# Optimization experiments

Hardware: AMD Instinct MI355X
Metric: run time of the kernel (lower is better)

Reference implementation:

```python
import jax, jax.numpy as jnp
import numpy as np

HID = 32          # PositionalEncodingFourier hidden_dim
PE_TEMP = 10000.0


def _layer_norm(x, w, b):
    m = jnp.mean(x, -1, keepdims=True)
    v = jnp.mean((x - m) ** 2, -1, keepdims=True)
    return (x - m) / jnp.sqrt(v + 1e-6) * w + b


def _dwconv(x, w, b):
    # x: (B,C,H,W), w: (C,1,3,3) depthwise
    y = jax.lax.conv_general_dilated(x, w, (1, 1), 'SAME',
                                     feature_group_count=x.shape[1],
                                     dimension_numbers=('NCHW', 'OIHW', 'NCHW'))
    return y + b[None, :, None, None]


def _pos_embed(B, H, W, pw, pb):
    scale = 2 * np.pi
    eps = 1e-6
    dim_t = PE_TEMP ** (2 * (jnp.arange(HID) // 2).astype(jnp.float32) / HID)

    def four(e):  # e: (M,) -> (M,HID), interleaved sin/cos
        p = e[:, None] / dim_t
        return jnp.stack([jnp.sin(p[:, 0::2]), jnp.cos(p[:, 1::2])], -1).reshape(e.shape[0], HID)

    ye = jnp.arange(1, H + 1, dtype=jnp.float32) / (H + eps) * scale
    xe = jnp.arange(1, W + 1, dtype=jnp.float32) / (W + eps) * scale
    py = jnp.broadcast_to(four(ye)[:, None, :], (H, W, HID))
    px = jnp.broadcast_to(four(xe)[None, :, :], (H, W, HID))
    pos = jnp.concatenate([py, px], -1) @ pw.T + pb     # (H,W,C)
    C = pos.shape[-1]
    return jnp.broadcast_to(pos[None], (B, H, W, C)).reshape(B, H * W, C)


def _l2norm(x):
    return x / jnp.maximum(jnp.linalg.norm(x, axis=-1, keepdims=True), 1e-12)


def setup_inputs() -> dict:
    key = jax.random.key(0)
    ks = jax.random.split(key, 10)
    B, C, H, W = 32, 384, 32, 32
    nh, hid = 6, 6 * C
    f32 = jnp.float32
    d = {
        'x': jax.random.normal(ks[0], (B, C, H, W), f32),
        'pos_w': 0.02 * jax.random.normal(ks[1], (C, 2 * HID), f32),
        'pos_b': jnp.zeros((C,), f32),
        'ln1_w': jnp.ones((C,), f32), 'ln1_b': jnp.zeros((C,), f32),
        'q_w': 0.02 * jax.random.normal(ks[2], (C, C), f32), 'q_b': jnp.zeros((C,), f32),
        'k_w': 0.02 * jax.random.normal(ks[3], (C, C), f32), 'k_b': jnp.zeros((C,), f32),
        'vc_w': 0.02 * jax.random.normal(ks[4], (C, C), f32), 'vc_b': jnp.zeros((C,), f32),
        'dw_w': 0.1 * jax.random.normal(ks[5], (C, 1, 3, 3), f32), 'dw_b': jnp.zeros((C,), f32),
        'bn_g': jnp.ones((C,), f32), 'bn_b': jnp.zeros((C,), f32),
        'bn_mean': jnp.zeros((C,), f32), 'bn_var': jnp.ones((C,), f32),
        'temp': jnp.ones((nh, 1, 1), f32),
        'proj_w': 0.02 * jax.random.normal(ks[6], (C, C), f32), 'proj_b': jnp.zeros((C,), f32),
        'gamma1': jnp.full((C,), 1e-6, f32),
        'ln2_w': jnp.ones((C,), f32), 'ln2_b': jnp.zeros((C,), f32),
        'mlp_w1': 0.02 * jax.random.normal(ks[7], (hid, C), f32), 'mlp_b1': jnp.zeros((hid,), f32),
        'mlp_dw': 0.1 * jax.random.normal(ks[8], (hid, 1, 3, 3), f32), 'mlp_db': jnp.zeros((hid,), f32),
        'mlp_w2': 0.02 * jax.random.normal(ks[9], (C, hid), f32), 'mlp_b2': jnp.zeros((C,), f32),
        'gamma2': jnp.full((C,), 1e-6, f32),
    }
    return d


def reference(x, pos_w, pos_b, ln1_w, ln1_b, q_w, q_b, k_w, k_b, vc_w, vc_b,
              dw_w, dw_b, bn_g, bn_b, bn_mean, bn_var, temp, proj_w, proj_b,
              gamma1, ln2_w, ln2_b, mlp_w1, mlp_b1, mlp_dw, mlp_db,
              mlp_w2, mlp_b2, gamma2):
    B, C, H, W = x.shape
    N = H * W
    nh = temp.shape[0]
    dh = C // nh

    xf = x.reshape(B, C, N).transpose(0, 2, 1)          # (B,N,C)
    xf = xf + _pos_embed(B, H, W, pos_w, pos_b)
    xn = _layer_norm(xf, ln1_w, ln1_b)                  # (B,N,C)
    xs = xn.transpose(0, 2, 1).reshape(B, C, H, W)      # spatial view for DWConv

    # --- GLGXCA: channel-wise cross-covariance attention ---
    q = (xn @ q_w.T + q_b).reshape(B, N, nh, dh).transpose(0, 2, 3, 1)  # (B,h,d,N)
    k = (xn @ k_w.T + k_b).reshape(B, N, nh, dh).transpose(0, 2, 3, 1)
    q = _l2norm(q)
    k = _l2norm(k)
    attn = jnp.einsum('bhdn,bhen->bhde', q, k) * temp   # (B,h,d,d)
    attn = jax.nn.softmax(attn, axis=-1)

    vg = _dwconv(xs, dw_w, dw_b)
    vg = (vg - bn_mean[None, :, None, None]) / jnp.sqrt(bn_var + 1e-5)[None, :, None, None] \
         * bn_g[None, :, None, None] + bn_b[None, :, None, None]
    vg = vg * jax.nn.sigmoid(vg)                        # SiLU
    vg = vg.transpose(0, 2, 3, 1).reshape(B, N, C)
    vc = xn @ vc_w.T + vc_b
    v = (vc * vg).reshape(B, N, nh, dh).transpose(0, 2, 3, 1)           # (B,h,d,N)

    xo = jnp.einsum('bhde,bhen->bhdn', attn, v)         # (B,h,d,N)
    xo = xo.transpose(0, 3, 1, 2).reshape(B, N, C)
    xo = xo @ proj_w.T + proj_b
    xo = xo.reshape(B, H, W, C).transpose(0, 3, 1, 2)   # (B,C,H,W)

    # --- residual 1 (faithful: torch does transpose(1,2).reshape on BCHW) ---
    xa = xo * gamma1[None, :, None, None]
    xa = jnp.swapaxes(xa, 1, 2).reshape(B, C, H, W)
    x = x + xa

    # --- MLP branch ---
    xn2 = _layer_norm(x.transpose(0, 2, 3, 1), ln2_w, ln2_b).transpose(0, 3, 1, 2)
    h1 = jnp.einsum('bchw,oc->bohw', xn2, mlp_w1) + mlp_b1[None, :, None, None]
    h1 = jax.nn.gelu(h1, approximate=False)
    h2 = jax.nn.gelu(_dwconv(h1, mlp_dw, mlp_db), approximate=False)
    h3 = jnp.einsum('bchw,oc->bohw', h2, mlp_w2) + mlp_b2[None, :, None, None]
    return x + h3 * gamma2[None, :, None, None]
```

## Files before the change

### kernel.cpp

```cpp
#include <hip/hip_runtime.h>
#include <cstdint>
#include <cstddef>
#include <cmath>

#define DI __device__ __forceinline__

typedef __attribute__((ext_vector_type(2))) float f32x2;
typedef __attribute__((ext_vector_type(4))) float f32x4;
typedef __attribute__((ext_vector_type(8))) __bf16 bf16x8;
typedef __attribute__((ext_vector_type(2))) unsigned short u16x2;
typedef __attribute__((ext_vector_type(4))) unsigned short u16x4;
typedef __attribute__((ext_vector_type(4))) unsigned int u32x4;

constexpr int B_ = 32, C_ = 384, N_ = 1024, HID2_ = 2304, QS_ = 1152;

DI unsigned short f2b(float f) {
  union { float f; unsigned int u; } v; v.f = f;
  unsigned int u = v.u;
  return (unsigned short)((u + 0x7FFFu + ((u >> 16) & 1u)) >> 16);
}
DI float b2f(unsigned short h) {
  union { unsigned int u; float f; } v; v.u = ((unsigned int)h) << 16;
  return v.f;
}
DI float sigmoid_f(float x) { return __builtin_amdgcn_rcpf(1.0f + __expf(-x)); }
DI float gelu_f(float x) { return x * sigmoid_f(1.702f * x); }

DI void gload_lds16(const void* g, void* l) {
  __builtin_amdgcn_global_load_lds(
      (const __attribute__((address_space(1))) void*)g,
      (__attribute__((address_space(3))) void*)l, 16, 0, 0);
}

#if __has_builtin(__builtin_amdgcn_cvt_pk_fp8_f32) && __has_builtin(__builtin_amdgcn_cvt_pk_f32_fp8)
#define HW_FP8 1
#else
#define HW_FP8 0
#endif

DI unsigned char f2e4_sw(float x) {
  float a = fabsf(x);
  unsigned char s = (x < 0.f) ? 0x80 : 0;
  if (!(a >= 0.0009765625f)) return s;
  if (a >= 448.f) return s | 0x7E;
  int e; float m = frexpf(a, &e);
  m *= 2.f; e -= 1;
  if (e < -6) {
    int q = (int)rintf(a * 512.f);
    if (q > 7) return s | 0x08;
    return s | (unsigned char)q;
  }
  int mi = (int)rintf((m - 1.f) * 8.f);
  if (mi == 8) { mi = 0; e += 1; }
  if (e > 8) return s | 0x7E;
  return s | (unsigned char)(((e + 7) << 3) | mi);
}
DI float e42f_sw(unsigned char h) {
  int e = (h >> 3) & 0xF, m = h & 7;
  float v;
  if (e == 0) v = (float)m * 0.001953125f;
  else { union { unsigned u; float f; } w; w.u = (unsigned)((e + 120) << 23) | ((unsigned)m << 20); v = w.f; }
  return (h & 0x80) ? -v : v;
}
DI unsigned char f2e4(float x) {
#if HW_FP8
  int r = __builtin_amdgcn_cvt_pk_fp8_f32(x, x, 0, false);
  return (unsigned char)(r & 0xFF);
#else
  return f2e4_sw(x);
#endif
}
DI unsigned int enc4(float a, float b, float c, float d) {
#if HW_FP8
  int r = 0;
  r = __builtin_amdgcn_cvt_pk_fp8_f32(a, b, r, false);
  r = __builtin_amdgcn_cvt_pk_fp8_f32(c, d, r, true);
  return (unsigned int)r;
#else
  return (unsigned)f2e4(a) | ((unsigned)f2e4(b) << 8) | ((unsigned)f2e4(c) << 16) | ((unsigned)f2e4(d) << 24);
#endif
}
DI void dec4(unsigned int v, float* o) {
#if HW_FP8
  f32x2 lo = __builtin_amdgcn_cvt_pk_f32_fp8((int)v, false);
  f32x2 hi = __builtin_amdgcn_cvt_pk_f32_fp8((int)v, true);
  o[0] = lo[0]; o[1] = lo[1]; o[2] = hi[0]; o[3] = hi[1];
#else
  o[0] = e42f_sw(v & 0xFF); o[1] = e42f_sw((v >> 8) & 0xFF);
  o[2] = e42f_sw((v >> 16) & 0xFF); o[3] = e42f_sw((v >> 24) & 0xFF);
#endif
}

__global__ void prep_k(const float* __restrict__ q_w, const float* __restrict__ k_w,
    const float* __restrict__ vc_w, const float* __restrict__ pj_w,
    const float* __restrict__ w1, const float* __restrict__ w2,
    const float* __restrict__ dw_w, const float* __restrict__ mdw,
    const float* __restrict__ q_b, const float* __restrict__ k_b, const float* __restrict__ v_b,
    unsigned short* __restrict__ WQKV, unsigned short* __restrict__ WP,
    unsigned char* __restrict__ W1, unsigned char* __restrict__ W2,
    float* __restrict__ DT1, float* __restrict__ DT2,
    float* __restrict__ BQKV, float* __restrict__ feat) {
  int i = blockIdx.x * 256 + threadIdx.x;
  if (i < 442368) {
    int o = i / 384, c = i % 384;
    float v = (o < 384) ? q_w[o * 384 + c] : (o < 768) ? k_w[(o - 384) * 384 + c]
                                                       : vc_w[(o - 768) * 384 + c];
    WQKV[i] = f2b(v); return;
  }
  i -= 442368;
  if (i < 147456) { WP[i] = f2b(pj_w[i]); return; }
  i -= 147456;
  if (i < 884736) { W1[i] = f2e4(w1[i]); return; }
  i -= 884736;
  if (i < 884736) { W2[i] = f2e4(w2[i]); return; }
  i -= 884736;
  if (i < 3456)  { int c = i / 9, k = i % 9; DT1[k * C_ + c] = dw_w[i]; return; }
  i -= 3456;
  if (i < 20736) { int c = i / 9, k = i % 9; DT2[k * HID2_ + c] = mdw[i]; return; }
  i -= 20736;
  if (i < 1152)  { BQKV[i] = (i < 384) ? q_b[i] : (i < 768) ? k_b[i - 384] : v_b[i - 768]; return; }
  i -= 1152;
  if (i < 65536) {
    int n = i >> 6, j = i & 63;
    int h = n >> 5, w = n & 31;
    const float scale = 6.283185307179586f;
    float e = (j < 32) ? (float)(h + 1) / (32.0f + 1e-6f) * scale
                       : (float)(w + 1) / (32.0f + 1e-6f) * scale;
    int jj = j & 31;
    float dt = powf(10000.0f, (float)(jj >> 1) * (1.0f / 16.0f));
    float arg = e / dt;
    feat[i] = (jj & 1) ? cosf(arg) : sinf(arg);
  }
}

__global__ __launch_bounds__(384) void pos_k(const float* __restrict__ feat,
    const float* __restrict__ pw, const float* __restrict__ pb, float* __restrict__ pos) {
  __shared__ float fs[64];
  int n = blockIdx.x, c = threadIdx.x;
  if (c < 64) fs[c] = feat[n * 64 + c];
  __syncthreads();
  float s = pb[c];
  #pragma unroll
  for (int j = 0; j < 64; ++j) s += fs[j] * pw[c * 64 + j];
  pos[(size_t)n * C_ + c] = s;
}

template<int HASPOS, int OUT8>
__global__ __launch_bounds__(256) void ln_k(const float* __restrict__ xin,
    const float* __restrict__ pos, const float* __restrict__ lw,
    const float* __restrict__ lb, unsigned short* __restrict__ outb,
    unsigned char* __restrict__ out8) {
  __shared__ float tile[C_ * 33];
  int bid = blockIdx.x;
  int b = bid >> 5, n0 = (bid & 31) << 5;
  int t = threadIdx.x;
  const float* xb = xin + (size_t)b * C_ * N_;
  #pragma unroll
  for (int i = 0; i < 48; ++i) {
    int f = t + 256 * i;
    int c = f >> 5, nn = f & 31;
    tile[c * 33 + nn] = xb[(size_t)c * N_ + n0 + nn];
  }
  __syncthreads();
  int wv = t >> 6, l = t & 63;
  for (int tk = 0; tk < 8; ++tk) {
    int tn = wv * 8 + tk;
    float v[6];
    #pragma unroll
    for (int i = 0; i < 6; ++i) {
      int c = l + 64 * i;
      float x = tile[c * 33 + tn];
      if (HASPOS) x += pos[(size_t)(n0 + tn) * C_ + c];
      v[i] = x;
    }
    float s = v[0] + v[1] + v[2] + v[3] + v[4] + v[5];
    #pragma unroll
    for (int m = 1; m < 64; m <<= 1) s += __shfl_xor(s, m);
    float mean = s * (1.0f / 384.0f);
    float q = 0.f;
    #pragma unroll
    for (int i = 0; i < 6; ++i) { float d = v[i] - mean; q += d * d; }
    #pragma unroll
    for (int m = 1; m < 64; m <<= 1) q += __shfl_xor(q, m);
    float rstd = rsqrtf(q * (1.0f / 384.0f) + 1e-6f);
    #pragma unroll
    for (int i = 0; i < 6; ++i) {
      int c = l + 64 * i;
      float val = (v[i] - mean) * rstd * lw[c] + lb[c];
      if (OUT8) out8[((size_t)b * N_ + n0 + tn) * C_ + c] = f2e4(val);
      else      outb[((size_t)b * N_ + n0 + tn) * C_ + c] = f2b(val);
    }
  }
}

template<int EPI>
__global__ __launch_bounds__(256) void gemm_k(const unsigned short* __restrict__ A,
    const unsigned short* __restrict__ Wt, const float* __restrict__ bias,
    unsigned short* __restrict__ outb, int M, int K, int O) {
  __shared__ __align__(16) unsigned short As[2][128 * 64];
  __shared__ __align__(16) unsigned short Bs[2][128 * 64];
  const int gx = gridDim.x;
  const int nwg = gx * gridDim.y;
  const int lid = blockIdx.y * gx + blockIdx.x;
  const int chunk = nwg >> 3;
  const int swz = (lid & 7) * chunk + (lid >> 3);
  const int m0 = (swz / gx) * 128, n0 = (swz % gx) * 128;
  const int t = threadIdx.x, l = t & 63, wv = t >> 6;
  const int wr = wv >> 1, wc = wv & 1;
  const int fr = l & 15, fq = l >> 4;
  const int arow = t >> 3;
  const int acsw = ((t & 7) ^ (arow & 7)) * 8;
  const unsigned short* Ag = A + (size_t)(m0 + arow) * K + acsw;
  const unsigned short* Bg = Wt + (size_t)(n0 + arow) * K + acsw;
  f32x4 acc[4][4];
  #pragma unroll
  for (int i = 0; i < 4; ++i)
    #pragma unroll
    for (int j = 0; j < 4; ++j) acc[i][j] = f32x4{0.f, 0.f, 0.f, 0.f};

  auto stage = [&](int buf, int k0) {
    char* Ad = (char*)&As[buf][0] + wv * 1024;
    char* Bd = (char*)&Bs[buf][0] + wv * 1024;
    #pragma unroll
    for (int s = 0; s < 4; ++s) {
      gload_lds16(Ag + (size_t)(s * 32) * K + k0, Ad + s * 4096);
      gload_lds16(Bg + (size_t)(s * 32) * K + k0, Bd + s * 4096);
    }
  };

  const int nt = K >> 6;
  stage(0, 0);
  for (int tt = 0; tt < nt; ++tt) {
    const int cur = tt & 1;
    if (tt + 1 < nt) {
      stage(cur ^ 1, (tt + 1) << 6);
      asm volatile("s_waitcnt vmcnt(8)" ::: "memory");
    } else {
      asm volatile("s_waitcnt vmcnt(0)" ::: "memory");
    }
    __builtin_amdgcn_s_barrier();
    #pragma unroll
    for (int kk = 0; kk < 2; ++kk) {
      bf16x8 af[4], bfr[4];
      #pragma unroll
      for (int mi = 0; mi < 4; ++mi) {
        int row = wr * 64 + mi * 16 + fr;
        af[mi] = *(const bf16x8*)((const char*)&As[cur][0] + row * 128 +
                                  ((((kk << 2) | fq) ^ (row & 7)) << 4));
      }
      #pragma unroll
      for (int ni = 0; ni < 4; ++ni) {
        int row = wc * 64 + ni * 16 + fr;
        bfr[ni] = *(const bf16x8*)((const char*)&Bs[cur][0] + row * 128 +
                                   ((((kk << 2) | fq) ^ (row & 7)) << 4));
      }
      #pragma unroll
      for (int mi = 0; mi < 4; ++mi)
        #pragma unroll
        for (int ni = 0; ni < 4; ++ni)
          acc[mi][ni] = __builtin_amdgcn_mfma_f32_16x16x32_bf16(af[mi], bfr[ni], acc[mi][ni], 0, 0, 0);
    }
    __builtin_amdgcn_s_barrier();
  }
  const int rb = fq * 4;
  #pragma unroll
  for (int mi = 0; mi < 4; ++mi) {
    #pragma unroll
    for (int ni = 0; ni < 4; ++ni) {
      int col = n0 + wc * 64 + ni * 16 + fr;
      float bv = bias[col];
      #pragma unroll
      for (int j = 0; j < 4; ++j) {
        int row = m0 + wr * 64 + mi * 16 + rb + j;
        outb[(size_t)row * O + col] = f2b(acc[mi][ni][j] + bv);
      }
    }
  }
}

__global__ __launch_bounds__(256) void fc1_8_k(const unsigned char* __restrict__ A,
    const unsigned char* __restrict__ Wt, const float* __restrict__ bias,
    unsigned char* __restrict__ outb8, int K, int O) {
  __shared__ __align__(16) unsigned char As[2][128 * 128];
  __shared__ __align__(16) unsigned char Bs[2][128 * 128];
  const int gx = gridDim.x;
  const int nwg = gx * gridDim.y;
  const int lid = blockIdx.y * gx + blockIdx.x;
  const int chunk = nwg >> 3;
  const int swz = (lid & 7) * chunk + (lid >> 3);
  const int m0 = (swz / gx) * 128, n0 = (swz % gx) * 128;
  const int t = threadIdx.x, l = t & 63, wv = t >> 6;
  const int wr = wv >> 1, wc = wv & 1;
  const int fr = l & 15, fq = l >> 4;
  const int arow = t >> 3;
  const int acsw = ((t & 7) ^ (arow & 7)) * 16;
  const unsigned char* Ag = A + (size_t)(m0 + arow) * K + acsw;
  const unsigned char* Bg = Wt + (size_t)(n0 + arow) * K + acsw;
  f32x4 acc[4][4];
  #pragma unroll
  for (int i = 0; i < 4; ++i)
    #pragma unroll
    for (int j = 0; j < 4; ++j) acc[i][j] = f32x4{0.f, 0.f, 0.f, 0.f};

  auto stage = [&](int buf, int k0) {
    char* Ad = (char*)&As[buf][0] + wv * 1024;
    char* Bd = (char*)&Bs[buf][0] + wv * 1024;
    #pragma unroll
    for (int s = 0; s < 4; ++s) {
      gload_lds16(Ag + (size_t)(s * 32) * K + k0, Ad + s * 4096);
      gload_lds16(Bg + (size_t)(s * 32) * K + k0, Bd + s * 4096);
    }
  };

  const int nt = K >> 7;
  stage(0, 0);
  for (int tt = 0; tt < nt; ++tt) {
    const int cur = tt & 1;
    if (tt + 1 < nt) {
      stage(cur ^ 1, (tt + 1) << 7);
      asm volatile("s_waitcnt vmcnt(8)" ::: "memory");
    } else {
      asm volatile("s_waitcnt vmcnt(0)" ::: "memory");
    }
    __builtin_amdgcn_s_barrier();
    #pragma unroll
    for (int kk = 0; kk < 4; ++kk) {
      const int slot = (kk << 1) | (fq >> 1);
      const int sub = (fq & 1) << 3;
      long af[4], bfr[4];
      #pragma unroll
      for (int mi = 0; mi < 4; ++mi) {
        int row = wr * 64 + mi * 16 + fr;
        af[mi] = *(const long*)((const char*)&As[cur][0] + row * 128 +
                                ((slot ^ (row & 7)) << 4) + sub);
      }
      #pragma unroll
      for (int ni = 0; ni < 4; ++ni) {
        int row = wc * 64 + ni * 16 + fr;
        bfr[ni] = *(const long*)((const char*)&Bs[cur][0] + row * 128 +
                                 ((slot ^ (row & 7)) << 4) + sub);
      }
      #pragma unroll
      for (int mi = 0; mi < 4; ++mi)
        #pragma unroll
        for (int ni = 0; ni < 4; ++ni)
          acc[mi][ni] = __builtin_amdgcn_mfma_f32_16x16x32_fp8_fp8(af[mi], bfr[ni], acc[mi][ni], 0, 0, 0);
    }
    __builtin_amdgcn_s_barrier();
  }
  const int rb = fq * 4;
  #pragma unroll
  for (int mi = 0; mi < 4; ++mi) {
    #pragma unroll
    for (int ni = 0; ni < 4; ++ni) {
      int col = n0 + wc * 64 + ni * 16 + fr;
      float bv = bias[col];
      #pragma unroll
      for (int j = 0; j < 4; ++j) {
        int row = m0 + wr * 64 + mi * 16 + rb + j;
        outb8[(size_t)row * O + col] = f2e4(gelu_f(acc[mi][ni][j] + bv));
      }
    }
  }
}

__global__ __launch_bounds__(256) void fc2t8_k(const unsigned char* __restrict__ W2b,
    const unsigned char* __restrict__ H2, const float* __restrict__ b2,
    const float* __restrict__ g2, float* __restrict__ out, int bofs) {
  __shared__ __align__(16) unsigned char As[2][128 * 128];
  __shared__ __align__(16) unsigned char Bs[2][128 * 128];
  const int K = HID2_;
  const int nwg = 8 * gridDim.y;
  const int lid = blockIdx.y * 8 + blockIdx.x;
  const int chunk = nwg >> 3;
  const int swz = (lid & 7) * chunk + (lid >> 3);
  const int n0 = (swz & 7) * 128;
  const int y2 = swz >> 3;
  const int img = y2 / 3, m0 = (y2 % 3) * 128;
  const int t = threadIdx.x, l = t & 63, wv = t >> 6;
  const int wr = wv >> 1, wc = wv & 1;
  const int fr = l & 15, fq = l >> 4;
  const int arow = t >> 3;
  const int acsw = ((t & 7) ^ (arow & 7)) * 16;
  const unsigned char* Ag = W2b + (size_t)(m0 + arow) * K + acsw;
  const unsigned char* Bg = H2 + ((size_t)img * N_ + n0 + arow) * K + acsw;
  f32x4 acc[4][4];
  #pragma unroll
  for (int i = 0; i < 4; ++i)
    #pragma unroll
    for (int j = 0; j < 4; ++j) acc[i][j] = f32x4{0.f, 0.f, 0.f, 0.f};

  auto stage = [&](int buf, int k0) {
    char* Ad = (char*)&As[buf][0] + wv * 1024;
    char* Bd = (char*)&Bs[buf][0] + wv * 1024;
    #pragma unroll
    for (int s = 0; s < 4; ++s) {
      gload_lds16(Ag + (size_t)(s * 32) * K + k0, Ad + s * 4096);
      gload_lds16(Bg + (size_t)(s * 32) * K + k0, Bd + s * 4096);
    }
  };

  const int nt = K >> 7;
  stage(0, 0);
  for (int tt = 0; tt < nt; ++tt) {
    const int cur = tt & 1;
    if (tt + 1 < nt) {
      stage(cur ^ 1, (tt + 1) << 7);
      asm volatile("s_waitcnt vmcnt(8)" ::: "memory");
    } else {
      asm volatile("s_waitcnt vmcnt(0)" ::: "memory");
    }
    __builtin_amdgcn_s_barrier();
    #pragma unroll
    for (int kk = 0; kk < 4; ++kk) {
      const int slot = (kk << 1) | (fq >> 1);
      const int sub = (fq & 1) << 3;
      long af[4], bfr[4];
      #pragma unroll
      for (int mi = 0; mi < 4; ++mi) {
        int row = wr * 64 + mi * 16 + fr;
        af[mi] = *(const long*)((const char*)&As[cur][0] + row * 128 +
                                ((slot ^ (row & 7)) << 4) + sub);
      }
      #pragma unroll
      for (int ni = 0; ni < 4; ++ni) {
        int row = wc * 64 + ni * 16 + fr;
        bfr[ni] = *(const long*)((const char*)&Bs[cur][0] + row * 128 +
                                 ((slot ^ (row & 7)) << 4) + sub);
      }
      #pragma unroll
      for (int mi = 0; mi < 4; ++mi)
        #pragma unroll
        for (int ni = 0; ni < 4; ++ni)
          acc[mi][ni] = __builtin_amdgcn_mfma_f32_16x16x32_fp8_fp8(af[mi], bfr[ni], acc[mi][ni], 0, 0, 0);
    }
    __builtin_amdgcn_s_barrier();
  }
  const int rb = fq * 4;
  const size_t obase = ((size_t)(img + bofs) * C_) << 10;
  #pragma unroll
  for (int mi = 0; mi < 4; ++mi) {
    #pragma unroll
    for (int j = 0; j < 4; ++j) {
      int row = m0 + wr * 64 + mi * 16 + rb + j;
      float bv = b2[row], gv = g2[row];
      #pragma unroll
      for (int ni = 0; ni < 4; ++ni) {
        int col = n0 + wc * 64 + ni * 16 + fr;
        size_t oi = obase + ((size_t)row << 10) + col;
        out[oi] = out[oi] + gv * (acc[mi][ni][j] + bv);
      }
    }
  }
}

__global__ __launch_bounds__(256) void attn_k(const unsigned short* __restrict__ qkv,
    const float* __restrict__ temp, unsigned short* __restrict__ attnbf) {
  __shared__ __align__(16) float Qs[32][68];
  __shared__ __align__(16) float Ks[32][68];
  __shared__ float qinv_s[64], kinv_s[64];
  const int bid = blockIdx.x;
  const int b = bid / 6, h = bid % 6;
  const int t = threadIdx.x;
  const unsigned short* qb = qkv + (size_t)b * N_ * QS_ + h * 64;
  const unsigned short* kb = qb + 384;
  const int li = t >> 4, ld = (t & 15) * 4;
  const int d0 = (t >> 4) * 4, e0 = (t & 15) * 4;
  float acc[4][4] = {};
  float ssq = 0.0f;
  for (int n0 = 0; n0 < N_; n0 += 32) {
    __syncthreads();
    #pragma unroll
    for (int rr = 0; rr < 2; ++rr) {
      int i = li + rr * 16;
      u16x4 qv = *(const u16x4*)(qb + (size_t)(n0 + i) * QS_ + ld);
      u16x4 kv = *(const u16x4*)(kb + (size_t)(n0 + i) * QS_ + ld);
      #pragma unroll
      for (int j = 0; j < 4; ++j) { Qs[i][ld + j] = b2f(qv[j]); Ks[i][ld + j] = b2f(kv[j]); }
    }
    __syncthreads();
    if (t < 64) {
      #pragma unroll
      for (int i = 0; i < 32; ++i) { float x = Qs[i][t]; ssq += x * x; }
    } else if (t < 128) {
      #pragma unroll
      for (int i = 0; i < 32; ++i) { float x = Ks[i][t - 64]; ssq += x * x; }
    }
    #pragma unroll
    for (int i = 0; i < 32; ++i) {
      f32x4 qv = *(const f32x4*)&Qs[i][d0];
      f32x4 kv = *(const f32x4*)&Ks[i][e0];
      #pragma unroll
      for (int di = 0; di < 4; ++di)
        #pragma unroll
        for (int ei = 0; ei < 4; ++ei) acc[di][ei] += qv[di] * kv[ei];
    }
  }
  if (t < 64) { float nr = sqrtf(ssq); qinv_s[t] = 1.0f / fmaxf(nr, 1e-12f); }
  else if (t < 128) { float nr = sqrtf(ssq); kinv_s[t - 64] = 1.0f / fmaxf(nr, 1e-12f); }
  __syncthreads();
  const float tp = temp[h];
  #pragma unroll
  for (int di = 0; di < 4; ++di) {
    int d = d0 + di;
    float vals[4];
    #pragma unroll
    for (int ei = 0; ei < 4; ++ei) vals[ei] = acc[di][ei] * qinv_s[d] * kinv_s[e0 + ei] * tp;
    float mx = fmaxf(fmaxf(vals[0], vals[1]), fmaxf(vals[2], vals[3]));
    #pragma unroll
    for (int m = 1; m < 16; m <<= 1) mx = fmaxf(mx, __shfl_xor(mx, m));
    float ex[4], s = 0.f;
    #pragma unroll
    for (int ei = 0; ei < 4; ++ei) { ex[ei] = __expf(vals[ei] - mx); s += ex[ei]; }
    #pragma unroll
    for (int m = 1; m < 16; m <<= 1) s += __shfl_xor(s, m);
    float inv = __builtin_amdgcn_rcpf(s);
    u16x4 ov;
    #pragma unroll
    for (int ei = 0; ei < 4; ++ei) ov[ei] = f2b(ex[ei] * inv);
    *(u16x4*)(attnbf + ((size_t)(b * 6 + h) * 64 + d) * 64 + e0) = ov;
  }
}

__global__ __launch_bounds__(192) void dwconv1_k(const unsigned short* __restrict__ xn,
    const float* __restrict__ dwt, const float* __restrict__ dwb,
    const float* __restrict__ bng, const float* __restrict__ bnb,
    const float* __restrict__ bnm, const float* __restrict__ bnv,
    unsigned short* __restrict__ qkv) {
  const int c0 = threadIdx.x * 4;
  const int h = blockIdx.y >> 2;
  const int w0 = (blockIdx.y & 3) * 8 + threadIdx.y * 4;
  const int b = blockIdx.z;
  const unsigned short* xb = xn + ((size_t)b * N_ + h * 32) * C_ + c0;
  f32x4 acc[4] = {};
  #pragma unroll
  for (int dy = -1; dy <= 1; ++dy) {
    int hh = h + dy;
    if (hh < 0 || hh >= 32) continue;
    f32x4 xf[6];
    #pragma unroll
    for (int j = 0; j < 6; ++j) {
      int ww = w0 - 1 + j;
      if (ww >= 0 && ww < 32) {
        u16x4 xv = *(const u16x4*)(xb + (dy * 32 + ww) * C_);
        xf[j] = f32x4{b2f(xv[0]), b2f(xv[1]), b2f(xv[2]), b2f(xv[3])};
      } else xf[j] = f32x4{0.f, 0.f, 0.f, 0.f};
    }
    #pragma unroll
    for (int dx = 0; dx < 3; ++dx) {
      f32x4 wv = *(const f32x4*)(dwt + ((dy + 1) * 3 + dx) * C_ + c0);
      #pragma unroll
      for (int px = 0; px < 4; ++px)
        #pragma unroll
        for (int j = 0; j < 4; ++j) acc[px][j] += xf[dx + px][j] * wv[j];
    }
  }
  f32x4 dbv = *(const f32x4*)(dwb + c0);
  f32x4 mv = *(const f32x4*)(bnm + c0);
  f32x4 vv = *(const f32x4*)(bnv + c0);
  f32x4 gv = *(const f32x4*)(bng + c0);
  f32x4 bv = *(const f32x4*)(bnb + c0);
  f32x4 rs;
  #pragma unroll
  for (int j = 0; j < 4; ++j) rs[j] = rsqrtf(vv[j] + 1e-5f);
  unsigned short* vb = qkv + ((size_t)b * N_ + h * 32 + w0) * QS_ + 768 + c0;
  #pragma unroll
  for (int px = 0; px < 4; ++px) {
    u16x4 vcv = *(const u16x4*)(vb + px * QS_);
    u16x4 ov;
    #pragma unroll
    for (int j = 0; j < 4; ++j) {
      float u = (acc[px][j] + dbv[j] - mv[j]) * rs[j] * gv[j] + bv[j];
      float si = u * sigmoid_f(u);
      ov[j] = f2b(si * b2f(vcv[j]));
    }
    *(u16x4*)(vb + px * QS_) = ov;
  }
}

__global__ __launch_bounds__(256) void xo_k(const unsigned short* __restrict__ qkv,
    const unsigned short* __restrict__ attn, unsigned short* __restrict__ xo) {
  const int bid = blockIdx.x;
  const int b = bid / 96, r = bid % 96, h = r / 16, m0 = (r % 16) * 64;
  const int t = threadIdx.x, wv = t >> 6, l = t & 63;
  const int n0 = m0 + wv * 16;
  const int fr = l & 15, fk = (l >> 4) * 8;
  const unsigned short* vb = qkv + (size_t)b * N_ * QS_ + 768 + h * 64;
  const unsigned short* ab = attn + (size_t)(b * 6 + h) * 4096;
  f32x4 acc[4];
  #pragma unroll
  for (int i = 0; i < 4; ++i) acc[i] = f32x4{0.f, 0.f, 0.f, 0.f};
  #pragma unroll
  for (int k0 = 0; k0 < 64; k0 += 32) {
    bf16x8 af = *(const bf16x8*)(vb + (size_t)(n0 + fr) * QS_ + k0 + fk);
    #pragma unroll
    for (int ni = 0; ni < 4; ++ni) {
      bf16x8 bfr = *(const bf16x8*)(ab + (ni * 16 + fr) * 64 + k0 + fk);
      acc[ni] = __builtin_amdgcn_mfma_f32_16x16x32_bf16(af, bfr, acc[ni], 0, 0, 0);
    }
  }
  const int rb = (l >> 4) * 4;
  #pragma unroll
  for (int ni = 0; ni < 4; ++ni)
    #pragma unroll
    for (int j = 0; j < 4; ++j) {
      int row = n0 + rb + j;
      xo[((size_t)b * N_ + row) * C_ + h * 64 + ni * 16 + fr] = f2b(acc[ni][j]);
    }
}

__global__ __launch_bounds__(256) void resid1_k(const float* __restrict__ x,
    const unsigned short* __restrict__ y, const float* __restrict__ g1,
    float* __restrict__ xnew) {
  __shared__ unsigned short yp[32][36];
  __shared__ float g1s[32];
  const int bid = blockIdx.x;
  const int b = bid / C_, c2 = bid % C_;
  const int hsrc = c2 / 12, cs0 = (c2 % 12) * 32;
  const int t = threadIdx.x;
  {
    int wq = t >> 3, h4 = (t & 7) * 4;
    u16x4 vv = *(const u16x4*)(y + ((size_t)b * N_ + hsrc * 32 + wq) * C_ + cs0 + h4);
    *(u16x4*)&yp[wq][h4] = vv;
  }
  if (t < 32) g1s[t] = g1[cs0 + t];
  __syncthreads();
  int h2 = t >> 3, w0 = (t & 7) * 4;
  size_t base = (((size_t)b * C_ + c2) << 10) + h2 * 32 + w0;
  f32x4 xv = *(const f32x4*)(x + base);
  f32x4 ov;
  #pragma unroll
  for (int i = 0; i < 4; ++i) ov[i] = xv[i] + g1s[h2] * b2f(yp[w0 + i][h2]);
  *(f32x4*)(xnew + base) = ov;
}

__global__ __launch_bounds__(192) void dwconv2_k(const unsigned char* __restrict__ h1,
    const float* __restrict__ dwt, const float* __restrict__ dwb,
    unsigned char* __restrict__ h2) {
  const int c0 = (blockIdx.x * 192 + threadIdx.x) * 4;
  const int h = blockIdx.y >> 3, w0 = (blockIdx.y & 7) * 4;
  const int b = blockIdx.z;
  const unsigned char* xb = h1 + ((size_t)b * N_ + h * 32) * HID2_ + c0;
  f32x4 acc[4] = {};
  #pragma unroll
  for (int dy = -1; dy <= 1; ++dy) {
    int hh = h + dy;
    if (hh < 0 || hh >= 32) continue;
    f32x4 xf[6];
    #pragma unroll
    for (int j = 0; j < 6; ++j) {
      int ww = w0 - 1 + j;
      if (ww >= 0 && ww < 32) {
        unsigned int xv = *(const unsigned int*)(xb + (dy * 32 + ww) * HID2_);
        float d4[4]; dec4(xv, d4);
        xf[j] = f32x4{d4[0], d4[1], d4[2], d4[3]};
      } else xf[j] = f32x4{0.f, 0.f, 0.f, 0.f};
    }
    #pragma unroll
    for (int dx = 0; dx < 3; ++dx) {
      f32x4 wv = *(const f32x4*)(dwt + ((dy + 1) * 3 + dx) * HID2_ + c0);
      #pragma unroll
      for (int px = 0; px < 4; ++px)
        #pragma unroll
        for (int j = 0; j < 4; ++j) acc[px][j] += xf[dx + px][j] * wv[j];
    }
  }
  f32x4 dbv = *(const f32x4*)(dwb + c0);
  unsigned char* ob = h2 + ((size_t)b * N_ + h * 32 + w0) * HID2_ + c0;
  #pragma unroll
  for (int px = 0; px < 4; ++px) {
    unsigned int ov = enc4(gelu_f(acc[px][0] + dbv[0]), gelu_f(acc[px][1] + dbv[1]),
                           gelu_f(acc[px][2] + dbv[2]), gelu_f(acc[px][3] + dbv[3]));
    *(unsigned int*)(ob + px * HID2_) = ov;
  }
}

extern "C" void kernel_launch(void* const* d_in, const int* in_sizes, int n_in,
                              void* d_out, int out_size, void* d_ws, size_t ws_size,
                              hipStream_t stream) {
  (void)in_sizes; (void)n_in; (void)out_size;
  const float* x    = (const float*)d_in[0];
  const float* posw = (const float*)d_in[1];
  const float* posb = (const float*)d_in[2];
  const float* ln1w = (const float*)d_in[3];
  const float* ln1b = (const float*)d_in[4];
  const float* q_w  = (const float*)d_in[5];
  const float* q_b  = (const float*)d_in[6];
  const float* k_w  = (const float*)d_in[7];
  const float* k_b  = (const float*)d_in[8];
  const float* v_w  = (const float*)d_in[9];
  const float* v_b  = (const float*)d_in[10];
  const float* dw_w = (const float*)d_in[11];
  const float* dw_b = (const float*)d_in[12];
  const float* bn_g = (const float*)d_in[13];
  const float* bn_b = (const float*)d_in[14];
  const float* bn_m = (const float*)d_in[15];
  const float* bn_v = (const float*)d_in[16];
  const float* temp = (const float*)d_in[17];
  const float* pj_w = (const float*)d_in[18];
  const float* pj_b = (const float*)d_in[19];
  const float* g1   = (const float*)d_in[20];
  const float* ln2w = (const float*)d_in[21];
  const float* ln2b = (const float*)d_in[22];
  const float* w1   = (const float*)d_in[23];
  const float* b1   = (const float*)d_in[24];
  const float* mdw  = (const float*)d_in[25];
  const float* mdb  = (const float*)d_in[26];
  const float* w2   = (const float*)d_in[27];
  const float* b2   = (const float*)d_in[28];
  const float* g2   = (const float*)d_in[29];
  float* out = (float*)d_out;

  char* ws = (char*)d_ws;
  size_t off = 0;
  auto alloc = [&](size_t bytes) { size_t o = off; off += (bytes + 255) & ~(size_t)255; return o; };
  const size_t TOK = (size_t)B_ * N_;
  const size_t BNC2 = TOK * C_ * 2;

  size_t oWQKV = alloc(442368 * 2), oWP = alloc(147456 * 2);
  size_t oW1 = alloc(884736), oW2 = alloc(884736);
  size_t oDT1 = alloc(9 * C_ * 4), oDT2 = alloc(9 * HID2_ * 4);
  size_t oBQKV = alloc(1152 * 4);
  size_t oFEAT = alloc(65536 * 4);
  size_t oPOS  = alloc((size_t)N_ * C_ * 4);
  size_t oATT  = alloc((size_t)B_ * 6 * 4096 * 2);
  size_t oXN2  = alloc(TOK * C_);
  size_t oQKV  = alloc(TOK * QS_ * 2);
  size_t oSA = alloc(BNC2), oSC = alloc(BNC2);

  const size_t perImg = (size_t)N_ * HID2_;
  size_t avail = (ws_size > oQKV + 512) ? (ws_size - oQKV - 512) : 0;
  int CH = (int)(avail / (2 * perImg));
  if (CH < 1) CH = 1;
  if (CH > 32) CH = 32;
  size_t oH1 = oQKV;
  size_t oH2 = oQKV + (size_t)CH * perImg;

  unsigned short* WQKV = (unsigned short*)(ws + oWQKV);
  unsigned short* WP = (unsigned short*)(ws + oWP);
  unsigned char* W1 = (unsigned char*)(ws + oW1);
  unsigned char* W2 = (unsigned char*)(ws + oW2);
  float* DT1 = (float*)(ws + oDT1);
  float* DT2 = (float*)(ws + oDT2);
  float* BQKV = (float*)(ws + oBQKV);
  float* FEAT = (float*)(ws + oFEAT);
  float* POS  = (float*)(ws + oPOS);
  unsigned short* ATT = (unsigned short*)(ws + oATT);
  unsigned char* XN2 = (unsigned char*)(ws + oXN2);
  unsigned short* QKV = (unsigned short*)(ws + oQKV);
  unsigned short* SA = (unsigned short*)(ws + oSA);
  unsigned short* SC = (unsigned short*)(ws + oSC);
  unsigned char* H1 = (unsigned char*)(ws + oH1);
  unsigned char* H2 = (unsigned char*)(ws + oH2);

  prep_k<<<9571, 256, 0, stream>>>(q_w, k_w, v_w, pj_w, w1, w2, dw_w, mdw,
                                   q_b, k_b, v_b, WQKV, WP, W1, W2, DT1, DT2, BQKV, FEAT);
  pos_k<<<1024, 384, 0, stream>>>(FEAT, posw, posb, POS);
  ln_k<1, 0><<<1024, 256, 0, stream>>>(x, POS, ln1w, ln1b, SA, nullptr);
  gemm_k<0><<<dim3(9, 256), 256, 0, stream>>>(SA, WQKV, BQKV, QKV, 32768, 384, 1152);
  attn_k<<<192, 256, 0, stream>>>(QKV, temp, ATT);
  dwconv1_k<<<dim3(1, 128, 32), dim3(96, 2), 0, stream>>>(SA, DT1, dw_b, bn_g, bn_b, bn_m, bn_v, QKV);
  xo_k<<<3072, 256, 0, stream>>>(QKV, ATT, SC);
  gemm_k<0><<<dim3(3, 256), 256, 0, stream>>>(SC, WP, pj_b, SA, 32768, 384, 384);
  resid1_k<<<12288, 256, 0, stream>>>(x, SA, g1, out);
  ln_k<0, 1><<<1024, 256, 0, stream>>>(out, nullptr, ln2w, ln2b, nullptr, XN2);
  for (int b0 = 0; b0 < B_; b0 += CH) {
    int cb = (b0 + CH <= B_) ? CH : (B_ - b0);
    const unsigned char* xn2c = XN2 + (size_t)b0 * N_ * C_;
    fc1_8_k<<<dim3(18, cb * 8), 256, 0, stream>>>(xn2c, W1, b1, H1, 384, 2304);
    dwconv2_k<<<dim3(3, 256, cb), 192, 0, stream>>>(H1, DT2, mdb, H2);
    fc2t8_k<<<dim3(8, 3 * cb), 256, 0, stream>>>(W2, H2, b2, g2, out, b0);
  }
}
```

Measured before the change: 467.8 us.

## Move attention branch (QKV, attn, xo, proj) from bf16 to fp8

Switches the QKV projection, attention matrix, value gating, attn@V and the output projection from bf16 storage and MFMA to fp8 e4m3 storage with fp8 MFMA. The bf16 GEMM kernel is replaced by the existing fp8 GEMM, now templated by epilogue (plain fp8, GELU fp8, bf16 output). The intent is to halve memory traffic for the attention-branch intermediates and to use the faster fp8 matrix instructions. In exchange it adds more quantization error to q/k normalization, softmax weights and the projection.

```diff
diff --git a/kernel.cpp b/kernel.cpp
--- a/kernel.cpp
+++ b/kernel.cpp
@@ -8,9 +8,7 @@
 typedef __attribute__((ext_vector_type(2))) float f32x2;
 typedef __attribute__((ext_vector_type(4))) float f32x4;
 typedef __attribute__((ext_vector_type(8))) __bf16 bf16x8;
-typedef __attribute__((ext_vector_type(2))) unsigned short u16x2;
 typedef __attribute__((ext_vector_type(4))) unsigned short u16x4;
-typedef __attribute__((ext_vector_type(4))) unsigned int u32x4;
 
 constexpr int B_ = 32, C_ = 384, N_ = 1024, HID2_ = 2304, QS_ = 1152;
 
@@ -96,7 +94,7 @@
     const float* __restrict__ w1, const float* __restrict__ w2,
     const float* __restrict__ dw_w, const float* __restrict__ mdw,
     const float* __restrict__ q_b, const float* __restrict__ k_b, const float* __restrict__ v_b,
-    unsigned short* __restrict__ WQKV, unsigned short* __restrict__ WP,
+    unsigned char* __restrict__ WQKV, unsigned char* __restrict__ WP,
     unsigned char* __restrict__ W1, unsigned char* __restrict__ W2,
     float* __restrict__ DT1, float* __restrict__ DT2,
     float* __restrict__ BQKV, float* __restrict__ feat) {
@@ -105,10 +103,10 @@
     int o = i / 384, c = i % 384;
     float v = (o < 384) ? q_w[o * 384 + c] : (o < 768) ? k_w[(o - 384) * 384 + c]
                                                        : vc_w[(o - 768) * 384 + c];
-    WQKV[i] = f2b(v); return;
+    WQKV[i] = f2e4(v); return;
   }
   i -= 442368;
-  if (i < 147456) { WP[i] = f2b(pj_w[i]); return; }
+  if (i < 147456) { WP[i] = f2e4(pj_w[i]); return; }
   i -= 147456;
   if (i < 884736) { W1[i] = f2e4(w1[i]); return; }
   i -= 884736;
@@ -145,11 +143,10 @@
   pos[(size_t)n * C_ + c] = s;
 }
 
-template<int HASPOS, int OUT8>
+template<int HASPOS>
 __global__ __launch_bounds__(256) void ln_k(const float* __restrict__ xin,
     const float* __restrict__ pos, const float* __restrict__ lw,
-    const float* __restrict__ lb, unsigned short* __restrict__ outb,
-    unsigned char* __restrict__ out8) {
+    const float* __restrict__ lb, unsigned char* __restrict__ out8) {
   __shared__ float tile[C_ * 33];
   int bid = blockIdx.x;
   int b = bid >> 5, n0 = (bid & 31) << 5;
@@ -186,101 +183,16 @@
     #pragma unroll
     for (int i = 0; i < 6; ++i) {
       int c = l + 64 * i;
-      float val = (v[i] - mean) * rstd * lw[c] + lb[c];
-      if (OUT8) out8[((size_t)b * N_ + n0 + tn) * C_ + c] = f2e4(val);
-      else      outb[((size_t)b * N_ + n0 + tn) * C_ + c] = f2b(val);
+      out8[((size_t)b * N_ + n0 + tn) * C_ + c] = f2e4((v[i] - mean) * rstd * lw[c] + lb[c]);
     }
   }
 }
 
 template<int EPI>
-__global__ __launch_bounds__(256) void gemm_k(const unsigned short* __restrict__ A,
-    const unsigned short* __restrict__ Wt, const float* __restrict__ bias,
-    unsigned short* __restrict__ outb, int M, int K, int O) {
-  __shared__ __align__(16) unsigned short As[2][128 * 64];
-  __shared__ __align__(16) unsigned short Bs[2][128 * 64];
-  const int gx = gridDim.x;
-  const int nwg = gx * gridDim.y;
-  const int lid = blockIdx.y * gx + blockIdx.x;
-  const int chunk = nwg >> 3;
-  const int swz = (lid & 7) * chunk + (lid >> 3);
-  const int m0 = (swz / gx) * 128, n0 = (swz % gx) * 128;
-  const int t = threadIdx.x, l = t & 63, wv = t >> 6;
-  const int wr = wv >> 1, wc = wv & 1;
-  const int fr = l & 15, fq = l >> 4;
-  const int arow = t >> 3;
-  const int acsw = ((t & 7) ^ (arow & 7)) * 8;
-  const unsigned short* Ag = A + (size_t)(m0 + arow) * K + acsw;
-  const unsigned short* Bg = Wt + (size_t)(n0 + arow) * K + acsw;
-  f32x4 acc[4][4];
-  #pragma unroll
-  for (int i = 0; i < 4; ++i)
-    #pragma unroll
-    for (int j = 0; j < 4; ++j) acc[i][j] = f32x4{0.f, 0.f, 0.f, 0.f};
-
-  auto stage = [&](int buf, int k0) {
-    char* Ad = (char*)&As[buf][0] + wv * 1024;
-    char* Bd = (char*)&Bs[buf][0] + wv * 1024;
-    #pragma unroll
-    for (int s = 0; s < 4; ++s) {
-      gload_lds16(Ag + (size_t)(s * 32) * K + k0, Ad + s * 4096);
-      gload_lds16(Bg + (size_t)(s * 32) * K + k0, Bd + s * 4096);
-    }
-  };
-
-  const int nt = K >> 6;
-  stage(0, 0);
-  for (int tt = 0; tt < nt; ++tt) {
-    const int cur = tt & 1;
-    if (tt + 1 < nt) {
-      stage(cur ^ 1, (tt + 1) << 6);
-      asm volatile("s_waitcnt vmcnt(8)" ::: "memory");
-    } else {
-      asm volatile("s_waitcnt vmcnt(0)" ::: "memory");
-    }
-    __builtin_amdgcn_s_barrier();
-    #pragma unroll
-    for (int kk = 0; kk < 2; ++kk) {
-      bf16x8 af[4], bfr[4];
-      #pragma unroll
-      for (int mi = 0; mi < 4; ++mi) {
-        int row = wr * 64 + mi * 16 + fr;
-        af[mi] = *(const bf16x8*)((const char*)&As[cur][0] + row * 128 +
-                                  ((((kk << 2) | fq) ^ (row & 7)) << 4));
-      }
-      #pragma unroll
-      for (int ni = 0; ni < 4; ++ni) {
-        int row = wc * 64 + ni * 16 + fr;
-        bfr[ni] = *(const bf16x8*)((const char*)&Bs[cur][0] + row * 128 +
-                                   ((((kk << 2) | fq) ^ (row & 7)) << 4));
-      }
-      #pragma unroll
-      for (int mi = 0; mi < 4; ++mi)
-        #pragma unroll
-        for (int ni = 0; ni < 4; ++ni)
-          acc[mi][ni] = __builtin_amdgcn_mfma_f32_16x16x32_bf16(af[mi], bfr[ni], acc[mi][ni], 0, 0, 0);
-    }
-    __builtin_amdgcn_s_barrier();
-  }
-  const int rb = fq * 4;
-  #pragma unroll
-  for (int mi = 0; mi < 4; ++mi) {
-    #pragma unroll
-    for (int ni = 0; ni < 4; ++ni) {
-      int col = n0 + wc * 64 + ni * 16 + fr;
-      float bv = bias[col];
-      #pragma unroll
-      for (int j = 0; j < 4; ++j) {
-        int row = m0 + wr * 64 + mi * 16 + rb + j;
-        outb[(size_t)row * O + col] = f2b(acc[mi][ni][j] + bv);
-      }
-    }
-  }
-}
-
-__global__ __launch_bounds__(256) void fc1_8_k(const unsigned char* __restrict__ A,
+__global__ __launch_bounds__(256) void gemm8_k(const unsigned char* __restrict__ A,
     const unsigned char* __restrict__ Wt, const float* __restrict__ bias,
-    unsigned char* __restrict__ outb8, int K, int O) {
+    unsigned char* __restrict__ out8, unsigned short* __restrict__ outb,
+    int K, int O) {
   __shared__ __align__(16) unsigned char As[2][128 * 128];
   __shared__ __align__(16) unsigned char Bs[2][128 * 128];
   const int gx = gridDim.x;
@@ -358,7 +270,10 @@
       #pragma unroll
       for (int j = 0; j < 4; ++j) {
         int row = m0 + wr * 64 + mi * 16 + rb + j;
-        outb8[(size_t)row * O + col] = f2e4(gelu_f(acc[mi][ni][j] + bv));
+        float val = acc[mi][ni][j] + bv;
+        if (EPI == 0)      out8[(size_t)row * O + col] = f2e4(val);
+        else if (EPI == 1) out8[(size_t)row * O + col] = f2e4(gelu_f(val));
+        else               outb[(size_t)row * O + col] = f2b(val);
       }
     }
   }
@@ -454,16 +369,16 @@
   }
 }
 
-__global__ __launch_bounds__(256) void attn_k(const unsigned short* __restrict__ qkv,
-    const float* __restrict__ temp, unsigned short* __restrict__ attnbf) {
+__global__ __launch_bounds__(256) void attn_k(const unsigned char* __restrict__ qkv,
+    const float* __restrict__ temp, unsigned char* __restrict__ attn8) {
   __shared__ __align__(16) float Qs[32][68];
   __shared__ __align__(16) float Ks[32][68];
   __shared__ float qinv_s[64], kinv_s[64];
   const int bid = blockIdx.x;
   const int b = bid / 6, h = bid % 6;
   const int t = threadIdx.x;
-  const unsigned short* qb = qkv + (size_t)b * N_ * QS_ + h * 64;
-  const unsigned short* kb = qb + 384;
+  const unsigned char* qb = qkv + (size_t)b * N_ * QS_ + h * 64;
+  const unsigned char* kb = qb + 384;
   const int li = t >> 4, ld = (t & 15) * 4;
   const int d0 = (t >> 4) * 4, e0 = (t & 15) * 4;
   float acc[4][4] = {};
@@ -473,10 +388,12 @@
     #pragma unroll
     for (int rr = 0; rr < 2; ++rr) {
       int i = li + rr * 16;
-      u16x4 qv = *(const u16x4*)(qb + (size_t)(n0 + i) * QS_ + ld);
-      u16x4 kv = *(const u16x4*)(kb + (size_t)(n0 + i) * QS_ + ld);
-      #pragma unroll
-      for (int j = 0; j < 4; ++j) { Qs[i][ld + j] = b2f(qv[j]); Ks[i][ld + j] = b2f(kv[j]); }
+      unsigned int qv = *(const unsigned int*)(qb + (size_t)(n0 + i) * QS_ + ld);
+      unsigned int kv = *(const unsigned int*)(kb + (size_t)(n0 + i) * QS_ + ld);
+      float qd[4], kd[4];
+      dec4(qv, qd); dec4(kv, kd);
+      #pragma unroll
+      for (int j = 0; j < 4; ++j) { Qs[i][ld + j] = qd[j]; Ks[i][ld + j] = kd[j]; }
     }
     __syncthreads();
     if (t < 64) {
@@ -515,23 +432,21 @@
     #pragma unroll
     for (int m = 1; m < 16; m <<= 1) s += __shfl_xor(s, m);
     float inv = __builtin_amdgcn_rcpf(s);
-    u16x4 ov;
-    #pragma unroll
-    for (int ei = 0; ei < 4; ++ei) ov[ei] = f2b(ex[ei] * inv);
-    *(u16x4*)(attnbf + ((size_t)(b * 6 + h) * 64 + d) * 64 + e0) = ov;
-  }
-}
-
-__global__ __launch_bounds__(192) void dwconv1_k(const unsigned short* __restrict__ xn,
+    unsigned int ov = enc4(ex[0] * inv, ex[1] * inv, ex[2] * inv, ex[3] * inv);
+    *(unsigned int*)(attn8 + ((size_t)(b * 6 + h) * 64 + d) * 64 + e0) = ov;
+  }
+}
+
+__global__ __launch_bounds__(192) void dwconv1_k(const unsigned char* __restrict__ xn,
     const float* __restrict__ dwt, const float* __restrict__ dwb,
     const float* __restrict__ bng, const float* __restrict__ bnb,
     const float* __restrict__ bnm, const float* __restrict__ bnv,
-    unsigned short* __restrict__ qkv) {
+    unsigned char* __restrict__ qkv) {
   const int c0 = threadIdx.x * 4;
   const int h = blockIdx.y >> 2;
   const int w0 = (blockIdx.y & 3) * 8 + threadIdx.y * 4;
   const int b = blockIdx.z;
-  const unsigned short* xb = xn + ((size_t)b * N_ + h * 32) * C_ + c0;
+  const unsigned char* xb = xn + ((size_t)b * N_ + h * 32) * C_ + c0;
   f32x4 acc[4] = {};
   #pragma unroll
   for (int dy = -1; dy <= 1; ++dy) {
@@ -542,8 +457,9 @@
     for (int j = 0; j < 6; ++j) {
       int ww = w0 - 1 + j;
       if (ww >= 0 && ww < 32) {
-        u16x4 xv = *(const u16x4*)(xb + (dy * 32 + ww) * C_);
-        xf[j] = f32x4{b2f(xv[0]), b2f(xv[1]), b2f(xv[2]), b2f(xv[3])};
+        unsigned int xv = *(const unsigned int*)(xb + (dy * 32 + ww) * C_);
+        float d4[4]; dec4(xv, d4);
+        xf[j] = f32x4{d4[0], d4[1], d4[2], d4[3]};
       } else xf[j] = f32x4{0.f, 0.f, 0.f, 0.f};
     }
     #pragma unroll
@@ -563,49 +479,50 @@
   f32x4 rs;
   #pragma unroll
   for (int j = 0; j < 4; ++j) rs[j] = rsqrtf(vv[j] + 1e-5f);
-  unsigned short* vb = qkv + ((size_t)b * N_ + h * 32 + w0) * QS_ + 768 + c0;
+  unsigned char* vb = qkv + ((size_t)b * N_ + h * 32 + w0) * QS_ + 768 + c0;
   #pragma unroll
   for (int px = 0; px < 4; ++px) {
-    u16x4 vcv = *(const u16x4*)(vb + px * QS_);
-    u16x4 ov;
+    unsigned int vcv = *(const unsigned int*)(vb + px * QS_);
+    float vd[4]; dec4(vcv, vd);
+    float o4[4];
     #pragma unroll
     for (int j = 0; j < 4; ++j) {
       float u = (acc[px][j] + dbv[j] - mv[j]) * rs[j] * gv[j] + bv[j];
       float si = u * sigmoid_f(u);
-      ov[j] = f2b(si * b2f(vcv[j]));
-    }
-    *(u16x4*)(vb + px * QS_) = ov;
-  }
-}
-
-__global__ __launch_bounds__(256) void xo_k(const unsigned short* __restrict__ qkv,
-    const unsigned short* __restrict__ attn, unsigned short* __restrict__ xo) {
+      o4[j] = si * vd[j];
+    }
+    *(unsigned int*)(vb + px * QS_) = enc4(o4[0], o4[1], o4[2], o4[3]);
+  }
+}
+
+__global__ __launch_bounds__(256) void xo_k(const unsigned char* __restrict__ qkv,
+    const unsigned char* __restrict__ attn, unsigned char* __restrict__ xo) {
   const int bid = blockIdx.x;
   const int b = bid / 96, r = bid % 96, h = r / 16, m0 = (r % 16) * 64;
   const int t = threadIdx.x, wv = t >> 6, l = t & 63;
   const int n0 = m0 + wv * 16;
-  const int fr = l & 15, fk = (l >> 4) * 8;
-  const unsigned short* vb = qkv + (size_t)b * N_ * QS_ + 768 + h * 64;
-  const unsigned short* ab = attn + (size_t)(b * 6 + h) * 4096;
+  const int fr = l & 15, fq = l >> 4;
+  const unsigned char* vb = qkv + (size_t)b * N_ * QS_ + 768 + h * 64;
+  const unsigned char* ab = attn + (size_t)(b * 6 + h) * 4096;
   f32x4 acc[4];
   #pragma unroll
   for (int i = 0; i < 4; ++i) acc[i] = f32x4{0.f, 0.f, 0.f, 0.f};
   #pragma unroll
   for (int k0 = 0; k0 < 64; k0 += 32) {
-    bf16x8 af = *(const bf16x8*)(vb + (size_t)(n0 + fr) * QS_ + k0 + fk);
+    long af = *(const long*)(vb + (size_t)(n0 + fr) * QS_ + k0 + fq * 8);
     #pragma unroll
     for (int ni = 0; ni < 4; ++ni) {
-      bf16x8 bfr = *(const bf16x8*)(ab + (ni * 16 + fr) * 64 + k0 + fk);
-      acc[ni] = __builtin_amdgcn_mfma_f32_16x16x32_bf16(af, bfr, acc[ni], 0, 0, 0);
-    }
-  }
-  const int rb = (l >> 4) * 4;
+      long bfr = *(const long*)(ab + (ni * 16 + fr) * 64 + k0 + fq * 8);
+      acc[ni] = __builtin_amdgcn_mfma_f32_16x16x32_fp8_fp8(af, bfr, acc[ni], 0, 0, 0);
+    }
+  }
+  const int rb = fq * 4;
   #pragma unroll
   for (int ni = 0; ni < 4; ++ni)
     #pragma unroll
     for (int j = 0; j < 4; ++j) {
       int row = n0 + rb + j;
-      xo[((size_t)b * N_ + row) * C_ + h * 64 + ni * 16 + fr] = f2b(acc[ni][j]);
+      xo[((size_t)b * N_ + row) * C_ + h * 64 + ni * 16 + fr] = f2e4(acc[ni][j]);
     }
 }
 
@@ -715,18 +632,19 @@
   size_t off = 0;
   auto alloc = [&](size_t bytes) { size_t o = off; off += (bytes + 255) & ~(size_t)255; return o; };
   const size_t TOK = (size_t)B_ * N_;
-  const size_t BNC2 = TOK * C_ * 2;
-
-  size_t oWQKV = alloc(442368 * 2), oWP = alloc(147456 * 2);
+
+  size_t oWQKV = alloc(442368), oWP = alloc(147456);
   size_t oW1 = alloc(884736), oW2 = alloc(884736);
   size_t oDT1 = alloc(9 * C_ * 4), oDT2 = alloc(9 * HID2_ * 4);
   size_t oBQKV = alloc(1152 * 4);
   size_t oFEAT = alloc(65536 * 4);
   size_t oPOS  = alloc((size_t)N_ * C_ * 4);
-  size_t oATT  = alloc((size_t)B_ * 6 * 4096 * 2);
+  size_t oATT  = alloc((size_t)B_ * 6 * 4096);
   size_t oXN2  = alloc(TOK * C_);
-  size_t oQKV  = alloc(TOK * QS_ * 2);
-  size_t oSA = alloc(BNC2), oSC = alloc(BNC2);
+  size_t oQKV  = alloc(TOK * QS_);
+  size_t oXN = alloc(TOK * C_);
+  size_t oSC = alloc(TOK * C_);
+  size_t oSA = alloc(TOK * C_ * 2);
 
   const size_t perImg = (size_t)N_ * HID2_;
   size_t avail = (ws_size > oQKV + 512) ? (ws_size - oQKV - 512) : 0;
@@ -736,8 +654,8 @@
   size_t oH1 = oQKV;
   size_t oH2 = oQKV + (size_t)CH * perImg;
 
-  unsigned short* WQKV = (unsigned short*)(ws + oWQKV);
-  unsigned short* WP = (unsigned short*)(ws + oWP);
+  unsigned char* WQKV = (unsigned char*)(ws + oWQKV);
+  unsigned char* WP = (unsigned char*)(ws + oWP);
   unsigned char* W1 = (unsigned char*)(ws + oW1);
   unsigned char* W2 = (unsigned char*)(ws + oW2);
   float* DT1 = (float*)(ws + oDT1);
@@ -745,29 +663,30 @@
   float* BQKV = (float*)(ws + oBQKV);
   float* FEAT = (float*)(ws + oFEAT);
   float* POS  = (float*)(ws + oPOS);
-  unsigned short* ATT = (unsigned short*)(ws + oATT);
+  unsigned char* ATT = (unsigned char*)(ws + oATT);
   unsigned char* XN2 = (unsigned char*)(ws + oXN2);
-  unsigned short* QKV = (unsigned short*)(ws + oQKV);
+  unsigned char* QKV = (unsigned char*)(ws + oQKV);
+  unsigned char* XN = (unsigned char*)(ws + oXN);
+  unsigned char* SC = (unsigned char*)(ws + oSC);
   unsigned short* SA = (unsigned short*)(ws + oSA);
-  unsigned short* SC = (unsigned short*)(ws + oSC);
   unsigned char* H1 = (unsigned char*)(ws + oH1);
   unsigned char* H2 = (unsigned char*)(ws + oH2);
 
   prep_k<<<9571, 256, 0, stream>>>(q_w, k_w, v_w, pj_w, w1, w2, dw_w, mdw,
                                    q_b, k_b, v_b, WQKV, WP, W1, W2, DT1, DT2, BQKV, FEAT);
   pos_k<<<1024, 384, 0, stream>>>(FEAT, posw, posb, POS);
-  ln_k<1, 0><<<1024, 256, 0, stream>>>(x, POS, ln1w, ln1b, SA, nullptr);
-  gemm_k<0><<<dim3(9, 256), 256, 0, stream>>>(SA, WQKV, BQKV, QKV, 32768, 384, 1152);
+  ln_k<1><<<1024, 256, 0, stream>>>(x, POS, ln1w, ln1b, XN);
+  gemm8_k<0><<<dim3(9, 256), 256, 0, stream>>>(XN, WQKV, BQKV, QKV, nullptr, 384, 1152);
   attn_k<<<192, 256, 0, stream>>>(QKV, temp, ATT);
-  dwconv1_k<<<dim3(1, 128, 32), dim3(96, 2), 0, stream>>>(SA, DT1, dw_b, bn_g, bn_b, bn_m, bn_v, QKV);
+  dwconv1_k<<<dim3(1, 128, 32), dim3(96, 2), 0, stream>>>(XN, DT1, dw_b, bn_g, bn_b, bn_m, bn_v, QKV);
   xo_k<<<3072, 256, 0, stream>>>(QKV, ATT, SC);
-  gemm_k<0><<<dim3(3, 256), 256, 0, stream>>>(SC, WP, pj_b, SA, 32768, 384, 384);
+  gemm8_k<2><<<dim3(3, 256), 256, 0, stream>>>(SC, WP, pj_b, nullptr, SA, 384, 384);
   resid1_k<<<12288, 256, 0, stream>>>(x, SA, g1, out);
-  ln_k<0, 1><<<1024, 256, 0, stream>>>(out, nullptr, ln2w, ln2b, nullptr, XN2);
+  ln_k<0><<<1024, 256, 0, stream>>>(out, nullptr, ln2w, ln2b, XN2);
   for (int b0 = 0; b0 < B_; b0 += CH) {
     int cb = (b0 + CH <= B_) ? CH : (B_ - b0);
     const unsigned char* xn2c = XN2 + (size_t)b0 * N_ * C_;
-    fc1_8_k<<<dim3(18, cb * 8), 256, 0, stream>>>(xn2c, W1, b1, H1, 384, 2304);
+    gemm8_k<1><<<dim3(18, cb * 8), 256, 0, stream>>>(xn2c, W1, b1, H1, nullptr, 384, 2304);
     dwconv2_k<<<dim3(3, 256, cb), 192, 0, stream>>>(H1, DT2, mdb, H2);
     fc2t8_k<<<dim3(8, 3 * cb), 256, 0, stream>>>(W2, H2, b2, g2, out, b0);
   }
```

Measured after the change: 452.6 us. -3.3%, faster.
